# Kernel tuning notes

Measured on AMD Instinct MI355X. Metric: run time of the kernel, lower is better.

Reference implementation:

```python
import jax, jax.numpy as jnp
import numpy as np

E = 512        # audio_embd == video_embd
HID = 640      # hidden_dim
NH = 10        # n_heads
DK = HID // NH # 64
BTNK = 4
NUM_CLASSES = 527
B, L_AUD, L_VID = 4, 1024, 1024


def pos_encoding(L, d):
    pos = jnp.arange(L, dtype=jnp.float32)[:, None]
    div = jnp.exp(jnp.arange(0, d, 2, dtype=jnp.float32) * (-np.log(10000.0) / d))
    pe = jnp.zeros((L, d), dtype=jnp.float32)
    pe = pe.at[:, 0::2].set(jnp.sin(pos * div))
    pe = pe.at[:, 1::2].set(jnp.cos(pos * div))
    return pe


def layernorm(x, g, b, eps=1e-5):
    m = jnp.mean(x, axis=-1, keepdims=True)
    v = jnp.var(x, axis=-1, keepdims=True)
    return (x - m) * jax.lax.rsqrt(v + eps) * g + b


def setup_inputs() -> dict:
    key = jax.random.key(0)
    ks = jax.random.split(key, 16)
    s = 0.02
    return {
        "audio_feat": jax.random.normal(ks[0], (B, L_AUD, E), jnp.float32),
        "video_feat": jax.random.normal(ks[1], (B, L_VID, E), jnp.float32),
        "audio_tok": s * jax.random.normal(ks[2], (1, 1, E), jnp.float32),
        "video_tok": s * jax.random.normal(ks[3], (1, 1, E), jnp.float32),
        "btnk_toks": s * jax.random.normal(ks[4], (1, BTNK, E), jnp.float32),
        "Wk": s * jax.random.normal(ks[5], (E, HID), jnp.float32),
        "bk": jnp.zeros((HID,), jnp.float32),
        "Wq": s * jax.random.normal(ks[6], (E, HID), jnp.float32),
        "bq": jnp.zeros((HID,), jnp.float32),
        "Wv": s * jax.random.normal(ks[7], (E, HID), jnp.float32),
        "bv": jnp.zeros((HID,), jnp.float32),
        "ln_g": jnp.ones((HID,), jnp.float32),
        "ln_b": jnp.zeros((HID,), jnp.float32),
        "Wap": s * jax.random.normal(ks[8], (HID, NUM_CLASSES), jnp.float32),
        "bap": jnp.zeros((NUM_CLASSES,), jnp.float32),
        "Wvp": s * jax.random.normal(ks[9], (HID, NUM_CLASSES), jnp.float32),
        "bvp": jnp.zeros((NUM_CLASSES,), jnp.float32),
    }


def reference(audio_feat, video_feat, audio_tok, video_tok, btnk_toks,
              Wk, bk, Wq, bq, Wv, bv, ln_g, ln_b, Wap, bap, Wvp, bvp):
    b, La = audio_feat.shape[:2]
    Lv = video_feat.shape[1]
    # layout: [audio (La), aud_cls (1), bottleneck (BTNK), video (Lv), vid_cls (1)]
    feats = jnp.concatenate([
        audio_feat,
        jnp.broadcast_to(audio_tok, (b, 1, E)),
        jnp.broadcast_to(btnk_toks, (b, BTNK, E)),
        video_feat,
        jnp.broadcast_to(video_tok, (b, 1, E)),
    ], axis=1)
    L = feats.shape[1]
    feats = feats + pos_encoding(L, E)[None]  # dropout is identity at eval

    k = (feats @ Wk + bk).reshape(b, L, NH, DK)
    q = (feats @ Wq + bq).reshape(b, L, NH, DK)
    v = (feats @ Wv + bv).reshape(b, L, NH, DK)

    # NOTE: original computes einsum(k, q) and softmaxes over the q axis (-2).
    attn = jnp.einsum('bmhd,bnhd->bmnh', k, q) / np.sqrt(DK)
    # _get_btnk_mask(L) writes to rows/cols L+1:L+1+BTNK, which are out of
    # range for an (L, L) mask -> mask is all-False (upstream bug, kept faithful).
    attn = jax.nn.softmax(attn, axis=-2)
    out = jnp.einsum('bmnh,bnhd->bmhd', attn, v).reshape(b, L, HID)

    out = layernorm(out, ln_g, ln_b)
    aud_cls = out[:, 0]                 # indices replicate original exactly
    vid_cls = out[:, La + 1 + BTNK]
    aud_pred = aud_cls @ Wap + bap
    vid_pred = vid_cls @ Wvp + bvp
    return (aud_pred + vid_pred) / 2
```

## Files before the change

kernel.cpp:

```cpp
#include <hip/hip_runtime.h>
#include <cstddef>

#define E_DIM 512
#define HID   640
#define NH    10
#define DK    64
#define LTOT  2054
#define NCLS  527
#define NB    4
#define KC    (-0.0179889460390157f)

__device__ __forceinline__ float wave_reduce_sum_dpp(float x) {
    float t;
    t = __int_as_float(__builtin_amdgcn_update_dpp(0, __float_as_int(x), 0x111, 0xf, 0xf, false)); x += t;
    t = __int_as_float(__builtin_amdgcn_update_dpp(0, __float_as_int(x), 0x112, 0xf, 0xf, false)); x += t;
    t = __int_as_float(__builtin_amdgcn_update_dpp(0, __float_as_int(x), 0x114, 0xf, 0xe, false)); x += t;
    t = __int_as_float(__builtin_amdgcn_update_dpp(0, __float_as_int(x), 0x118, 0xf, 0xc, false)); x += t;
    t = __int_as_float(__builtin_amdgcn_update_dpp(0, __float_as_int(x), 0x142, 0xa, 0xf, false)); x += t;
    t = __int_as_float(__builtin_amdgcn_update_dpp(0, __float_as_int(x), 0x143, 0xc, 0xf, false)); x += t;
    return __int_as_float(__builtin_amdgcn_readlane(__float_as_int(x), 63));
}

__device__ __forceinline__ const float* row_src(int b, int n,
        const float* au, const float* vi, const float* at,
        const float* vt, const float* bt) {
    if (n < 1024) return au + ((size_t)b*1024 + n)*E_DIM;
    if (n == 1024) return at;
    if (n < 1029) return bt + (size_t)(n-1025)*E_DIM;
    if (n < 2053) return vi + ((size_t)b*1024 + (n-1029))*E_DIM;
    return vt;
}

__global__ __launch_bounds__(256) void ba_ku_kernel(
        const float* __restrict__ audio, const float* __restrict__ video,
        const float* __restrict__ Wk, const float* __restrict__ bk,
        const float* __restrict__ Wq, const float* __restrict__ bq,
        float* __restrict__ uws, float* __restrict__ cws) {
    int h = blockIdx.x, bm = blockIdx.y;
    int b = bm >> 1, m = bm & 1;
    int mrow = m ? 1029 : 0;
    const float* src = m ? (video + (size_t)b*1024*E_DIM)
                         : (audio + (size_t)b*1024*E_DIM);
    int t = threadIdx.x;
    __shared__ float frow[E_DIM];
    __shared__ __align__(16) float kl[DK];
    __shared__ float red[4][DK];
    for (int i = t; i < E_DIM; i += 256) {
        float div = expf((float)(i & ~1) * KC);
        float arg = (float)mrow * div;
        float pe  = (i & 1) ? cosf(arg) : sinf(arg);
        frow[i] = src[i] + pe;
    }
    __syncthreads();
    int d = t & 63, es = t >> 6;
    const float* wkcol = Wk + (size_t)(h*DK) + d;
    float part = 0.f;
    #pragma unroll 8
    for (int e = es*128; e < es*128 + 128; ++e)
        part = fmaf(frow[e], wkcol[(size_t)e*HID], part);
    red[es][d] = part;
    __syncthreads();
    if (t < DK)
        kl[t] = bk[h*DK + t] + red[0][t] + red[1][t] + red[2][t] + red[3][t];
    __syncthreads();
    #pragma unroll
    for (int s = 0; s < 2; ++s) {
        int e = s*256 + t;
        const float4* wq4 = (const float4*)(Wq + (size_t)e*HID + h*DK);
        const float4* k4  = (const float4*)kl;
        float acc = 0.f;
        #pragma unroll
        for (int d4 = 0; d4 < 16; ++d4) {
            float4 w = wq4[d4]; float4 kk = k4[d4];
            acc = fmaf(w.x,kk.x, fmaf(w.y,kk.y, fmaf(w.z,kk.z, fmaf(w.w,kk.w, acc))));
        }
        uws[((size_t)bm*NH + h)*E_DIM + e] = acc * 0.125f;
    }
    if (t < 64) {
        float prod = (t < DK) ? bq[h*DK + t] * kl[t] : 0.f;
        float tot = wave_reduce_sum_dpp(prod);
        if (t == 0) cws[bm*NH + h] = tot * 0.125f;
    }
}

__global__ __launch_bounds__(128) void ba_fused_kernel(
        const float* __restrict__ audio, const float* __restrict__ video,
        const float* __restrict__ atok, const float* __restrict__ vtok,
        const float* __restrict__ btnk,
        const float* __restrict__ uws, const float* __restrict__ cws,
        float* __restrict__ wpart, float* __restrict__ mcs,
        float* __restrict__ lcs, int nch, int crw) {
    int b = blockIdx.z, chunk = blockIdx.x, t = threadIdx.x;
    int w = t >> 6, lane = t & 63;
    int pbase = (blockIdx.y*2 + w)*2;
    int eb = lane*8;
    float4 u0[2], u1[2];
    float cadd[2];
    #pragma unroll
    for (int i = 0; i < 2; ++i) {
        const float4* up = (const float4*)(uws + (size_t)(b*20 + pbase + i)*E_DIM + eb);
        u0[i] = up[0]; u1[i] = up[1];
        cadd[i] = cws[b*20 + pbase + i];
    }
    int r0 = chunk*crw;
    float sn[4], cn[4], sd[4], cd[4];
    #pragma unroll
    for (int q = 0; q < 4; ++q) {
        float dv = expf((float)(eb + 2*q) * KC);
        sd[q] = sinf(dv); cd[q] = cosf(dv);
        float a = (float)r0 * dv;
        sn[q] = sinf(a); cn[q] = cosf(a);
    }
    float m[2], l[2], acc[2][8];
    #pragma unroll
    for (int i = 0; i < 2; ++i) {
        m[i] = -1e30f; l[i] = 0.f;
        #pragma unroll
        for (int j = 0; j < 8; ++j) acc[i][j] = 0.f;
    }
    int rend = min(r0 + crw, LTOT);

#define ADV_ROT() { \
    _Pragma("unroll") \
    for (int q = 0; q < 4; ++q) { \
        float s2_ = fmaf(sn[q], cd[q],  cn[q]*sd[q]); \
        float c2_ = fmaf(cn[q], cd[q], -sn[q]*sd[q]); \
        sn[q] = s2_; cn[q] = c2_; } }

#define MAKE_FP(fp, x0, x1) { \
    (fp)[0]=(x0).x+sn[0]; (fp)[1]=(x0).y+cn[0]; (fp)[2]=(x0).z+sn[1]; (fp)[3]=(x0).w+cn[1]; \
    (fp)[4]=(x1).x+sn[2]; (fp)[5]=(x1).y+cn[2]; (fp)[6]=(x1).z+sn[3]; (fp)[7]=(x1).w+cn[3]; }

#define DOT8(res, fp, i) { \
    float a_; \
    a_ = (fp)[0]*u0[i].x; \
    a_ = fmaf((fp)[1], u0[i].y, a_); \
    a_ = fmaf((fp)[2], u0[i].z, a_); \
    a_ = fmaf((fp)[3], u0[i].w, a_); \
    a_ = fmaf((fp)[4], u1[i].x, a_); \
    a_ = fmaf((fp)[5], u1[i].y, a_); \
    a_ = fmaf((fp)[6], u1[i].z, a_); \
    a_ = fmaf((fp)[7], u1[i].w, a_); \
    (res) = a_; }

#define SOFT_UPD(i, sc, fp) { \
    if ((sc) > m[i]) { \
        float scale_ = __expf(m[i] - (sc)); \
        m[i] = (sc); \
        l[i] = fmaf(l[i], scale_, 1.f); \
        _Pragma("unroll") \
        for (int j = 0; j < 8; ++j) acc[i][j] = fmaf(acc[i][j], scale_, (fp)[j]); \
    } else { \
        float wg_ = __expf((sc) - m[i]); \
        l[i] += wg_; \
        _Pragma("unroll") \
        for (int j = 0; j < 8; ++j) acc[i][j] = fmaf(wg_, (fp)[j], acc[i][j]); } }

    int r = r0;
    for (; r + 3 < rend; r += 4) {
        const float* s0p = row_src(b, r,   audio, video, atok, vtok, btnk);
        const float* s1p = row_src(b, r+1, audio, video, atok, vtok, btnk);
        const float* s2p = row_src(b, r+2, audio, video, atok, vtok, btnk);
        const float* s3p = row_src(b, r+3, audio, video, atok, vtok, btnk);
        float4 x00 = *(const float4*)(s0p + eb), x01 = *(const float4*)(s0p + eb + 4);
        float4 x10 = *(const float4*)(s1p + eb), x11 = *(const float4*)(s1p + eb + 4);
        float4 x20 = *(const float4*)(s2p + eb), x21 = *(const float4*)(s2p + eb + 4);
        float4 x30 = *(const float4*)(s3p + eb), x31 = *(const float4*)(s3p + eb + 4);
        float fp0[8], fp1[8], fp2[8], fp3[8];
        MAKE_FP(fp0, x00, x01); ADV_ROT();
        MAKE_FP(fp1, x10, x11); ADV_ROT();
        MAKE_FP(fp2, x20, x21); ADV_ROT();
        MAKE_FP(fp3, x30, x31); ADV_ROT();
        float d0, d1, d2, d3, d4, d5, d6, d7;
        DOT8(d0, fp0, 0); DOT8(d1, fp0, 1);
        DOT8(d2, fp1, 0); DOT8(d3, fp1, 1);
        DOT8(d4, fp2, 0); DOT8(d5, fp2, 1);
        DOT8(d6, fp3, 0); DOT8(d7, fp3, 1);
        float sc0 = wave_reduce_sum_dpp(d0) + cadd[0];
        float sc1 = wave_reduce_sum_dpp(d1) + cadd[1];
        float sc2 = wave_reduce_sum_dpp(d2) + cadd[0];
        float sc3 = wave_reduce_sum_dpp(d3) + cadd[1];
        float sc4 = wave_reduce_sum_dpp(d4) + cadd[0];
        float sc5 = wave_reduce_sum_dpp(d5) + cadd[1];
        float sc6 = wave_reduce_sum_dpp(d6) + cadd[0];
        float sc7 = wave_reduce_sum_dpp(d7) + cadd[1];
        SOFT_UPD(0, sc0, fp0); SOFT_UPD(0, sc2, fp1);
        SOFT_UPD(0, sc4, fp2); SOFT_UPD(0, sc6, fp3);
        SOFT_UPD(1, sc1, fp0); SOFT_UPD(1, sc3, fp1);
        SOFT_UPD(1, sc5, fp2); SOFT_UPD(1, sc7, fp3);
    }
    for (; r < rend; ++r) {
        const float* s0p = row_src(b, r, audio, video, atok, vtok, btnk);
        float4 x00 = *(const float4*)(s0p + eb), x01 = *(const float4*)(s0p + eb + 4);
        float fp0[8];
        MAKE_FP(fp0, x00, x01); ADV_ROT();
        float d0, d1;
        DOT8(d0, fp0, 0); DOT8(d1, fp0, 1);
        float sc0 = wave_reduce_sum_dpp(d0) + cadd[0];
        float sc1 = wave_reduce_sum_dpp(d1) + cadd[1];
        SOFT_UPD(0, sc0, fp0);
        SOFT_UPD(1, sc1, fp0);
    }
    #pragma unroll
    for (int i = 0; i < 2; ++i) {
        float* dst = wpart + ((size_t)(b*20 + pbase + i)*nch + chunk)*E_DIM + eb;
        *(float4*)dst       = make_float4(acc[i][0], acc[i][1], acc[i][2], acc[i][3]);
        *(float4*)(dst + 4) = make_float4(acc[i][4], acc[i][5], acc[i][6], acc[i][7]);
    }
    float mv = (lane == 0) ? m[0] : m[1];
    float lv = (lane == 0) ? l[0] : l[1];
    if (lane < 2) {
        size_t ix = (size_t)(b*20 + pbase + lane)*nch + chunk;
        mcs[ix] = mv;
        lcs[ix] = lv;
    }
#undef ADV_ROT
#undef MAKE_FP
#undef DOT8
#undef SOFT_UPD
}

__global__ __launch_bounds__(1024) void ba_outraw_kernel(
        const float* __restrict__ wpart, const float* __restrict__ mcs,
        const float* __restrict__ lcs,
        const float* __restrict__ Wv, const float* __restrict__ bv,
        float* __restrict__ orow, int nch) {
    int h = blockIdx.x, bm = blockIdx.y, t = threadIdx.x;
    int b = bm >> 1, m = bm & 1, p = m*10 + h;
    __shared__ float ml[128], ll[128], coefs[128];
    __shared__ float Msh, invLsh;
    __shared__ float wh[E_DIM];
    __shared__ float sh[2][E_DIM];
    __shared__ float red[16][64];
    const float* mrow = mcs + (size_t)(b*20 + p)*nch;
    const float* lrow = lcs + (size_t)(b*20 + p)*nch;
    if (t < nch) { ml[t] = mrow[t]; ll[t] = lrow[t]; }
    __syncthreads();
    if (t < 64) {
        float mv = -1e30f;
        for (int c = t; c < nch; c += 64) mv = fmaxf(mv, ml[c]);
        #pragma unroll
        for (int off = 1; off < 64; off <<= 1) mv = fmaxf(mv, __shfl_xor(mv, off, 64));
        if (t == 0) Msh = mv;
    }
    __syncthreads();
    float M = Msh;
    if (t < 64) {
        float lv = 0.f;
        for (int c = t; c < nch; c += 64) lv += ll[c] * __expf(ml[c] - M);
        lv = wave_reduce_sum_dpp(lv);
        if (t == 0) invLsh = 1.0f / lv;
    }
    __syncthreads();
    if (t < nch) coefs[t] = __expf(ml[t] - M) * invLsh;
    __syncthreads();
    int e = t & 511, half = t >> 9;
    const float* basep = wpart + (size_t)(b*20 + p)*nch*E_DIM;
    float acc = 0.f;
    int c0 = half*(nch >> 1), c1 = c0 + (nch >> 1);
    for (int c = c0; c < c1; ++c)
        acc = fmaf(basep[(size_t)c*E_DIM + e], coefs[c], acc);
    sh[half][e] = acc;
    __syncthreads();
    if (t < E_DIM) wh[t] = sh[0][t] + sh[1][t];
    __syncthreads();
    int d = t & 63, es = t >> 6;
    float part = 0.f;
    #pragma unroll 8
    for (int e2 = es*32; e2 < es*32 + 32; ++e2)
        part = fmaf(wh[e2], Wv[(size_t)e2*HID + h*DK + d], part);
    red[es][d] = part;
    __syncthreads();
    if (t < 64) {
        float s = 0.f;
        #pragma unroll
        for (int i = 0; i < 16; ++i) s += red[i][t];
        orow[(size_t)bm*HID + h*DK + t] = bv[h*DK + t] + s;
    }
}

__global__ __launch_bounds__(512) void ba_lnpred_kernel(
        const float* __restrict__ orow,
        const float* __restrict__ g, const float* __restrict__ bb,
        const float* __restrict__ Wap, const float* __restrict__ bap,
        const float* __restrict__ Wvp, const float* __restrict__ bvp,
        float* __restrict__ out) {
    int b = blockIdx.y, t = threadIdx.x;
    const float* A = orow + (size_t)(2*b)*HID;
    const float* V = orow + (size_t)(2*b + 1)*HID;
    __shared__ float lnA[HID], lnV[HID];
    __shared__ float wred[4][8];
    __shared__ float psum[8][2][64];
    float sA = 0.f, qA = 0.f, sV = 0.f, qV = 0.f;
    for (int i = t; i < HID; i += 512) {
        float xa = A[i]; sA += xa; qA = fmaf(xa, xa, qA);
        float xv = V[i]; sV += xv; qV = fmaf(xv, xv, qV);
    }
    sA = wave_reduce_sum_dpp(sA); qA = wave_reduce_sum_dpp(qA);
    sV = wave_reduce_sum_dpp(sV); qV = wave_reduce_sum_dpp(qV);
    int w = t >> 6, lane = t & 63;
    if (lane == 0) { wred[0][w] = sA; wred[1][w] = qA; wred[2][w] = sV; wred[3][w] = qV; }
    __syncthreads();
    float tsA = 0.f, tqA = 0.f, tsV = 0.f, tqV = 0.f;
    #pragma unroll
    for (int i = 0; i < 8; ++i) {
        tsA += wred[0][i]; tqA += wred[1][i]; tsV += wred[2][i]; tqV += wred[3][i];
    }
    float meanA = tsA*(1.0f/HID), varA = tqA*(1.0f/HID) - meanA*meanA;
    float meanV = tsV*(1.0f/HID), varV = tqV*(1.0f/HID) - meanV*meanV;
    float rA = rsqrtf(varA + 1e-5f), rV = rsqrtf(varV + 1e-5f);
    for (int i = t; i < HID; i += 512) {
        float gg = g[i], bbv = bb[i];
        lnA[i] = (A[i] - meanA)*rA*gg + bbv;
        lnV[i] = (V[i] - meanV)*rV*gg + bbv;
    }
    __syncthreads();
    int c = blockIdx.x*64 + lane;
    int cc = (c < NCLS) ? c : (NCLS - 1);
    int j0 = w*80;
    float sa = 0.f, sv = 0.f;
    #pragma unroll 8
    for (int j = j0; j < j0 + 80; ++j) {
        sa = fmaf(lnA[j], Wap[(size_t)j*NCLS + cc], sa);
        sv = fmaf(lnV[j], Wvp[(size_t)j*NCLS + cc], sv);
    }
    psum[w][0][lane] = sa;
    psum[w][1][lane] = sv;
    __syncthreads();
    if (t < 64 && c < NCLS) {
        float ta = 0.f, tv = 0.f;
        #pragma unroll
        for (int i = 0; i < 8; ++i) { ta += psum[i][0][t]; tv += psum[i][1][t]; }
        out[(size_t)b*NCLS + c] = 0.5f*(ta + tv + bap[c] + bvp[c]);
    }
}

extern "C" void kernel_launch(void* const* d_in, const int* in_sizes, int n_in,
                              void* d_out, int out_size, void* d_ws, size_t ws_size,
                              hipStream_t stream) {
    const float* audio = (const float*)d_in[0];
    const float* video = (const float*)d_in[1];
    const float* atok  = (const float*)d_in[2];
    const float* vtok  = (const float*)d_in[3];
    const float* btnk  = (const float*)d_in[4];
    const float* Wk    = (const float*)d_in[5];
    const float* bk    = (const float*)d_in[6];
    const float* Wq    = (const float*)d_in[7];
    const float* bq    = (const float*)d_in[8];
    const float* Wv    = (const float*)d_in[9];
    const float* bv    = (const float*)d_in[10];
    const float* ln_g  = (const float*)d_in[11];
    const float* ln_b  = (const float*)d_in[12];
    const float* Wap   = (const float*)d_in[13];
    const float* bap   = (const float*)d_in[14];
    const float* Wvp   = (const float*)d_in[15];
    const float* bvp   = (const float*)d_in[16];
    float* out = (float*)d_out;
    float* ws  = (float*)d_ws;

    auto need = [](int nch) -> size_t {
        return (size_t)(8*NH*E_DIM) + 80
             + (size_t)NB*nch*20*E_DIM + 2*(size_t)NB*nch*20
             + 8*HID;
    };
    int nch = 40;
    if (ws_size >= need(128)*sizeof(float)) nch = 128;
    else if (ws_size >= need(64)*sizeof(float)) nch = 64;
    int crw = (LTOT + nch - 1) / nch;

    float* uws   = ws;
    float* cws   = uws + 8*NH*E_DIM;
    float* wpart = cws + 80;
    float* mcs   = wpart + (size_t)NB*nch*20*E_DIM;
    float* lcs   = mcs + (size_t)NB*nch*20;
    float* orw   = lcs + (size_t)NB*nch*20;

    ba_ku_kernel<<<dim3(NH, 8), 256, 0, stream>>>(audio, video, Wk, bk, Wq, bq, uws, cws);
    ba_fused_kernel<<<dim3(nch, 5, NB), 128, 0, stream>>>(audio, video, atok, vtok, btnk,
                                                          uws, cws, wpart, mcs, lcs, nch, crw);
    ba_outraw_kernel<<<dim3(NH, 8), 1024, 0, stream>>>(wpart, mcs, lcs, Wv, bv, orw, nch);
    ba_lnpred_kernel<<<dim3(9, NB), 512, 0, stream>>>(orw, ln_g, ln_b,
                                                      Wap, bap, Wvp, bvp, out);
}
```

Before: 162.2 us.

## Split online softmax into score, stats and weighted-sum passes

Replaces the fused online-softmax kernel with three kernels: one writes raw scores to a buffer, one computes the per-row max and inverse sum, and one accumulates softmax-weighted features across all 20 query rows per block. The bq·k constant is dropped because softmax is shift-invariant, and the final reduction becomes a plain sum. This removes the branchy rescaling in the inner loop and improves feature reuse in the weighted sum. The cost is two extra launches, a second pass over the input features and a round trip of the scores through memory.

```diff
diff --git a/kernel.cpp b/kernel.cpp
--- a/kernel.cpp
+++ b/kernel.cpp
@@ -9,6 +9,11 @@
 #define NCLS  527
 #define NB    4
 #define KC    (-0.0179889460390157f)
+#define SPITCH 2056
+#define NSLICE 64
+#define CRS   32
+#define NSCH  65
+#define CRWS  33
 
 __device__ __forceinline__ float wave_reduce_sum_dpp(float x) {
     float t;
@@ -34,8 +39,8 @@
 __global__ __launch_bounds__(256) void ba_ku_kernel(
         const float* __restrict__ audio, const float* __restrict__ video,
         const float* __restrict__ Wk, const float* __restrict__ bk,
-        const float* __restrict__ Wq, const float* __restrict__ bq,
-        float* __restrict__ uws, float* __restrict__ cws) {
+        const float* __restrict__ Wq,
+        float* __restrict__ uws) {
     int h = blockIdx.x, bm = blockIdx.y;
     int b = bm >> 1, m = bm & 1;
     int mrow = m ? 1029 : 0;
@@ -76,33 +81,25 @@
         }
         uws[((size_t)bm*NH + h)*E_DIM + e] = acc * 0.125f;
     }
-    if (t < 64) {
-        float prod = (t < DK) ? bq[h*DK + t] * kl[t] : 0.f;
-        float tot = wave_reduce_sum_dpp(prod);
-        if (t == 0) cws[bm*NH + h] = tot * 0.125f;
-    }
-}
-
-__global__ __launch_bounds__(128) void ba_fused_kernel(
+}
+
+__global__ __launch_bounds__(128) void ba_scores_kernel(
         const float* __restrict__ audio, const float* __restrict__ video,
         const float* __restrict__ atok, const float* __restrict__ vtok,
         const float* __restrict__ btnk,
-        const float* __restrict__ uws, const float* __restrict__ cws,
-        float* __restrict__ wpart, float* __restrict__ mcs,
-        float* __restrict__ lcs, int nch, int crw) {
+        const float* __restrict__ uws, float* __restrict__ S) {
     int b = blockIdx.z, chunk = blockIdx.x, t = threadIdx.x;
     int w = t >> 6, lane = t & 63;
     int pbase = (blockIdx.y*2 + w)*2;
     int eb = lane*8;
+    int r0 = chunk*CRS;
+    if (r0 >= LTOT) return;
     float4 u0[2], u1[2];
-    float cadd[2];
     #pragma unroll
     for (int i = 0; i < 2; ++i) {
         const float4* up = (const float4*)(uws + (size_t)(b*20 + pbase + i)*E_DIM + eb);
         u0[i] = up[0]; u1[i] = up[1];
-        cadd[i] = cws[b*20 + pbase + i];
-    }
-    int r0 = chunk*crw;
+    }
     float sn[4], cn[4], sd[4], cd[4];
     #pragma unroll
     for (int q = 0; q < 4; ++q) {
@@ -111,14 +108,7 @@
         float a = (float)r0 * dv;
         sn[q] = sinf(a); cn[q] = cosf(a);
     }
-    float m[2], l[2], acc[2][8];
-    #pragma unroll
-    for (int i = 0; i < 2; ++i) {
-        m[i] = -1e30f; l[i] = 0.f;
-        #pragma unroll
-        for (int j = 0; j < 8; ++j) acc[i][j] = 0.f;
-    }
-    int rend = min(r0 + crw, LTOT);
+    int rend = min(r0 + CRS, LTOT);
 
 #define ADV_ROT() { \
     _Pragma("unroll") \
@@ -143,19 +133,8 @@
     a_ = fmaf((fp)[7], u1[i].w, a_); \
     (res) = a_; }
 
-#define SOFT_UPD(i, sc, fp) { \
-    if ((sc) > m[i]) { \
-        float scale_ = __expf(m[i] - (sc)); \
-        m[i] = (sc); \
-        l[i] = fmaf(l[i], scale_, 1.f); \
-        _Pragma("unroll") \
-        for (int j = 0; j < 8; ++j) acc[i][j] = fmaf(acc[i][j], scale_, (fp)[j]); \
-    } else { \
-        float wg_ = __expf((sc) - m[i]); \
-        l[i] += wg_; \
-        _Pragma("unroll") \
-        for (int j = 0; j < 8; ++j) acc[i][j] = fmaf(wg_, (fp)[j], acc[i][j]); } }
-
+    float* S0 = S + (size_t)(b*20 + pbase)*SPITCH;
+    float* S1 = S + (size_t)(b*20 + pbase + 1)*SPITCH;
     int r = r0;
     for (; r + 3 < rend; r += 4) {
         const float* s0p = row_src(b, r,   audio, video, atok, vtok, btnk);
@@ -176,18 +155,20 @@
         DOT8(d2, fp1, 0); DOT8(d3, fp1, 1);
         DOT8(d4, fp2, 0); DOT8(d5, fp2, 1);
         DOT8(d6, fp3, 0); DOT8(d7, fp3, 1);
-        float sc0 = wave_reduce_sum_dpp(d0) + cadd[0];
-        float sc1 = wave_reduce_sum_dpp(d1) + cadd[1];
-        float sc2 = wave_reduce_sum_dpp(d2) + cadd[0];
-        float sc3 = wave_reduce_sum_dpp(d3) + cadd[1];
-        float sc4 = wave_reduce_sum_dpp(d4) + cadd[0];
-        float sc5 = wave_reduce_sum_dpp(d5) + cadd[1];
-        float sc6 = wave_reduce_sum_dpp(d6) + cadd[0];
-        float sc7 = wave_reduce_sum_dpp(d7) + cadd[1];
-        SOFT_UPD(0, sc0, fp0); SOFT_UPD(0, sc2, fp1);
-        SOFT_UPD(0, sc4, fp2); SOFT_UPD(0, sc6, fp3);
-        SOFT_UPD(1, sc1, fp0); SOFT_UPD(1, sc3, fp1);
-        SOFT_UPD(1, sc5, fp2); SOFT_UPD(1, sc7, fp3);
+        float a0 = wave_reduce_sum_dpp(d0);
+        float a1 = wave_reduce_sum_dpp(d1);
+        float b0 = wave_reduce_sum_dpp(d2);
+        float b1 = wave_reduce_sum_dpp(d3);
+        float c0 = wave_reduce_sum_dpp(d4);
+        float c1 = wave_reduce_sum_dpp(d5);
+        float e0 = wave_reduce_sum_dpp(d6);
+        float e1 = wave_reduce_sum_dpp(d7);
+        float4 v = (lane == 0) ? make_float4(a0, b0, c0, e0)
+                               : make_float4(a1, b1, c1, e1);
+        if (lane < 2) {
+            float* dst = (lane == 0) ? (S0 + r) : (S1 + r);
+            *(float4*)dst = v;
+        }
     }
     for (; r < rend; ++r) {
         const float* s0p = row_src(b, r, audio, video, atok, vtok, btnk);
@@ -196,70 +177,106 @@
         MAKE_FP(fp0, x00, x01); ADV_ROT();
         float d0, d1;
         DOT8(d0, fp0, 0); DOT8(d1, fp0, 1);
-        float sc0 = wave_reduce_sum_dpp(d0) + cadd[0];
-        float sc1 = wave_reduce_sum_dpp(d1) + cadd[1];
-        SOFT_UPD(0, sc0, fp0);
-        SOFT_UPD(1, sc1, fp0);
-    }
-    #pragma unroll
-    for (int i = 0; i < 2; ++i) {
-        float* dst = wpart + ((size_t)(b*20 + pbase + i)*nch + chunk)*E_DIM + eb;
-        *(float4*)dst       = make_float4(acc[i][0], acc[i][1], acc[i][2], acc[i][3]);
-        *(float4*)(dst + 4) = make_float4(acc[i][4], acc[i][5], acc[i][6], acc[i][7]);
-    }
-    float mv = (lane == 0) ? m[0] : m[1];
-    float lv = (lane == 0) ? l[0] : l[1];
-    if (lane < 2) {
-        size_t ix = (size_t)(b*20 + pbase + lane)*nch + chunk;
-        mcs[ix] = mv;
-        lcs[ix] = lv;
+        float a0 = wave_reduce_sum_dpp(d0);
+        float a1 = wave_reduce_sum_dpp(d1);
+        if (lane == 0) S0[r] = a0;
+        if (lane == 1) S1[r] = a1;
     }
 #undef ADV_ROT
 #undef MAKE_FP
 #undef DOT8
-#undef SOFT_UPD
+}
+
+__global__ void ba_stats_kernel(const float* __restrict__ S,
+                                float* __restrict__ Mws, float* __restrict__ Iws) {
+    int row = blockIdx.x, t = threadIdx.x;
+    const float* Sr = S + (size_t)row*SPITCH;
+    __shared__ float red[256];
+    float lm = -1e30f;
+    for (int i = t; i < LTOT; i += 256) lm = fmaxf(lm, Sr[i]);
+    red[t] = lm; __syncthreads();
+    for (int s = 128; s; s >>= 1) { if (t < s) red[t] = fmaxf(red[t], red[t+s]); __syncthreads(); }
+    float M = red[0]; __syncthreads();
+    float ls = 0.f;
+    for (int i = t; i < LTOT; i += 256) ls += __expf(Sr[i] - M);
+    red[t] = ls; __syncthreads();
+    for (int s = 128; s; s >>= 1) { if (t < s) red[t] += red[t+s]; __syncthreads(); }
+    if (t == 0) { Mws[row] = M; Iws[row] = 1.0f / red[0]; }
+}
+
+__global__ __launch_bounds__(256) void ba_wsum_kernel(
+        const float* __restrict__ audio, const float* __restrict__ video,
+        const float* __restrict__ atok, const float* __restrict__ vtok,
+        const float* __restrict__ btnk,
+        const float* __restrict__ S, const float* __restrict__ Mws,
+        const float* __restrict__ Iws, float* __restrict__ wpart) {
+    int b = blockIdx.y, sl = blockIdx.x, t = threadIdx.x;
+    int w = t >> 6, lane = t & 63;
+    int p0 = w*5, eb = lane*8;
+    float M[5], I[5];
+    #pragma unroll
+    for (int i = 0; i < 5; ++i) {
+        M[i] = Mws[b*20 + p0 + i];
+        I[i] = Iws[b*20 + p0 + i];
+    }
+    int r0 = sl*CRWS;
+    float sn[4], cn[4], sd[4], cd[4];
+    #pragma unroll
+    for (int q = 0; q < 4; ++q) {
+        float dv = expf((float)(eb + 2*q) * KC);
+        sd[q] = sinf(dv); cd[q] = cosf(dv);
+        float a = (float)r0 * dv;
+        sn[q] = sinf(a); cn[q] = cosf(a);
+    }
+    float acc[5][8];
+    #pragma unroll
+    for (int i = 0; i < 5; ++i)
+        #pragma unroll
+        for (int j = 0; j < 8; ++j) acc[i][j] = 0.f;
+    int rend = min(r0 + CRWS, LTOT);
+    for (int r = r0; r < rend; ++r) {
+        const float* src = row_src(b, r, audio, video, atok, vtok, btnk);
+        float4 f0 = *(const float4*)(src + eb);
+        float4 f1 = *(const float4*)(src + eb + 4);
+        float fp[8];
+        fp[0]=f0.x+sn[0]; fp[1]=f0.y+cn[0]; fp[2]=f0.z+sn[1]; fp[3]=f0.w+cn[1];
+        fp[4]=f1.x+sn[2]; fp[5]=f1.y+cn[2]; fp[6]=f1.z+sn[3]; fp[7]=f1.w+cn[3];
+        #pragma unroll
+        for (int q = 0; q < 4; ++q) {
+            float s2 = fmaf(sn[q], cd[q],  cn[q]*sd[q]);
+            float c2 = fmaf(cn[q], cd[q], -sn[q]*sd[q]);
+            sn[q] = s2; cn[q] = c2;
+        }
+        #pragma unroll
+        for (int i = 0; i < 5; ++i) {
+            float wgt = __expf(S[(size_t)(b*20 + p0 + i)*SPITCH + r] - M[i]) * I[i];
+            #pragma unroll
+            for (int j = 0; j < 8; ++j) acc[i][j] = fmaf(wgt, fp[j], acc[i][j]);
+        }
+    }
+    #pragma unroll
+    for (int i = 0; i < 5; ++i) {
+        float* dst = wpart + ((size_t)(b*20 + p0 + i)*NSLICE + sl)*E_DIM + eb;
+        *(float4*)dst       = make_float4(acc[i][0], acc[i][1], acc[i][2], acc[i][3]);
+        *(float4*)(dst + 4) = make_float4(acc[i][4], acc[i][5], acc[i][6], acc[i][7]);
+    }
 }
 
 __global__ __launch_bounds__(1024) void ba_outraw_kernel(
-        const float* __restrict__ wpart, const float* __restrict__ mcs,
-        const float* __restrict__ lcs,
+        const float* __restrict__ wpart,
         const float* __restrict__ Wv, const float* __restrict__ bv,
-        float* __restrict__ orow, int nch) {
+        float* __restrict__ orow) {
     int h = blockIdx.x, bm = blockIdx.y, t = threadIdx.x;
     int b = bm >> 1, m = bm & 1, p = m*10 + h;
-    __shared__ float ml[128], ll[128], coefs[128];
-    __shared__ float Msh, invLsh;
     __shared__ float wh[E_DIM];
     __shared__ float sh[2][E_DIM];
     __shared__ float red[16][64];
-    const float* mrow = mcs + (size_t)(b*20 + p)*nch;
-    const float* lrow = lcs + (size_t)(b*20 + p)*nch;
-    if (t < nch) { ml[t] = mrow[t]; ll[t] = lrow[t]; }
-    __syncthreads();
-    if (t < 64) {
-        float mv = -1e30f;
-        for (int c = t; c < nch; c += 64) mv = fmaxf(mv, ml[c]);
-        #pragma unroll
-        for (int off = 1; off < 64; off <<= 1) mv = fmaxf(mv, __shfl_xor(mv, off, 64));
-        if (t == 0) Msh = mv;
-    }
-    __syncthreads();
-    float M = Msh;
-    if (t < 64) {
-        float lv = 0.f;
-        for (int c = t; c < nch; c += 64) lv += ll[c] * __expf(ml[c] - M);
-        lv = wave_reduce_sum_dpp(lv);
-        if (t == 0) invLsh = 1.0f / lv;
-    }
-    __syncthreads();
-    if (t < nch) coefs[t] = __expf(ml[t] - M) * invLsh;
-    __syncthreads();
     int e = t & 511, half = t >> 9;
-    const float* basep = wpart + (size_t)(b*20 + p)*nch*E_DIM;
+    const float* basep = wpart + (size_t)(b*20 + p)*NSLICE*E_DIM;
     float acc = 0.f;
-    int c0 = half*(nch >> 1), c1 = c0 + (nch >> 1);
+    int c0 = half*(NSLICE/2), c1 = c0 + (NSLICE/2);
     for (int c = c0; c < c1; ++c)
-        acc = fmaf(basep[(size_t)c*E_DIM + e], coefs[c], acc);
+        acc += basep[(size_t)c*E_DIM + e];
     sh[half][e] = acc;
     __syncthreads();
     if (t < E_DIM) wh[t] = sh[0][t] + sh[1][t];
@@ -346,7 +363,6 @@
     const float* Wk    = (const float*)d_in[5];
     const float* bk    = (const float*)d_in[6];
     const float* Wq    = (const float*)d_in[7];
-    const float* bq    = (const float*)d_in[8];
     const float* Wv    = (const float*)d_in[9];
     const float* bv    = (const float*)d_in[10];
     const float* ln_g  = (const float*)d_in[11];
@@ -358,27 +374,20 @@
     float* out = (float*)d_out;
     float* ws  = (float*)d_ws;
 
-    auto need = [](int nch) -> size_t {
-        return (size_t)(8*NH*E_DIM) + 80
-             + (size_t)NB*nch*20*E_DIM + 2*(size_t)NB*nch*20
-             + 8*HID;
-    };
-    int nch = 40;
-    if (ws_size >= need(128)*sizeof(float)) nch = 128;
-    else if (ws_size >= need(64)*sizeof(float)) nch = 64;
-    int crw = (LTOT + nch - 1) / nch;
-
     float* uws   = ws;
-    float* cws   = uws + 8*NH*E_DIM;
-    float* wpart = cws + 80;
-    float* mcs   = wpart + (size_t)NB*nch*20*E_DIM;
-    float* lcs   = mcs + (size_t)NB*nch*20;
-    float* orw   = lcs + (size_t)NB*nch*20;
-
-    ba_ku_kernel<<<dim3(NH, 8), 256, 0, stream>>>(audio, video, Wk, bk, Wq, bq, uws, cws);
-    ba_fused_kernel<<<dim3(nch, 5, NB), 128, 0, stream>>>(audio, video, atok, vtok, btnk,
-                                                          uws, cws, wpart, mcs, lcs, nch, crw);
-    ba_outraw_kernel<<<dim3(NH, 8), 1024, 0, stream>>>(wpart, mcs, lcs, Wv, bv, orw, nch);
+    float* S     = uws + 8*NH*E_DIM;
+    float* Mws   = S + (size_t)80*SPITCH;
+    float* Iws   = Mws + 80;
+    float* wpart = Iws + 80;
+    float* orw   = wpart + (size_t)80*NSLICE*E_DIM;
+
+    ba_ku_kernel<<<dim3(NH, 8), 256, 0, stream>>>(audio, video, Wk, bk, Wq, uws);
+    ba_scores_kernel<<<dim3(NSCH, 5, NB), 128, 0, stream>>>(audio, video, atok, vtok,
+                                                            btnk, uws, S);
+    ba_stats_kernel<<<80, 256, 0, stream>>>(S, Mws, Iws);
+    ba_wsum_kernel<<<dim3(NSLICE, NB), 256, 0, stream>>>(audio, video, atok, vtok, btnk,
+                                                         S, Mws, Iws, wpart);
+    ba_outraw_kernel<<<dim3(NH, 8), 1024, 0, stream>>>(wpart, Wv, bv, orw);
     ba_lnpred_kernel<<<dim3(9, NB), 512, 0, stream>>>(orw, ln_g, ln_b,
                                                       Wap, bap, Wvp, bvp, out);
 }
```

Measured after the change: 168.7 us. 4.0% more time.
